# Kernel tuning notes

Hardware: AMD Instinct MI355X
Metric: run time of the kernel (lower is better)

Reference implementation:

```python
import jax, jax.numpy as jnp
import numpy as np

T, B, UNITS, ACTIONS = 128, 16, 128, 6
NORM_SCALE = float(np.sqrt(UNITS))  # norm_scale = sqrt(urnn_units)


def _conv(x, w, b, stride):
    y = jax.lax.conv_general_dilated(x, w, (stride, stride), 'VALID',
                                     dimension_numbers=('NCHW', 'OIHW', 'NCHW'))
    return jax.nn.relu(y + b[None, :, None, None])


def setup_inputs() -> dict:
    key = jax.random.key(0)
    ks = jax.random.split(key, 16)
    rn = lambda k, s, sc=0.05: jax.random.normal(k, s, jnp.float32) * sc
    return {
        'x': jax.random.uniform(ks[0], (T * B, 84, 84, 3), jnp.float32, 0.0, 255.0),
        'done': (jax.random.uniform(ks[1], (T * B,)) < 0.1).astype(jnp.float32),
        'urnn_state_real': jnp.ones((B, UNITS), jnp.float32),
        'urnn_state_imag': jnp.zeros((B, UNITS), jnp.float32),
        'conv1_w': rn(ks[2], (32, 3, 8, 8)), 'conv1_b': jnp.zeros((32,), jnp.float32),
        'conv2_w': rn(ks[3], (64, 32, 4, 4)), 'conv2_b': jnp.zeros((64,), jnp.float32),
        'conv3_w': rn(ks[4], (64, 64, 3, 3)), 'conv3_b': jnp.zeros((64,), jnp.float32),
        'fc_w': rn(ks[5], (3136, 512)), 'fc_b': jnp.zeros((512,), jnp.float32),
        'win_r': rn(ks[6], (512, UNITS)), 'win_i': rn(ks[7], (512, UNITS)),
        'wrec_r': rn(ks[8], (UNITS, UNITS)), 'wrec_i': rn(ks[9], (UNITS, UNITS)),
        'actor_w': rn(ks[10], (2 * UNITS, ACTIONS), 0.01), 'actor_b': jnp.zeros((ACTIONS,), jnp.float32),
        'critic_w': rn(ks[11], (2 * UNITS, 1)), 'critic_b': jnp.zeros((1,), jnp.float32),
    }


def reference(x, done, urnn_state_real, urnn_state_imag,
              conv1_w, conv1_b, conv2_w, conv2_b, conv3_w, conv3_b,
              fc_w, fc_b, win_r, win_i, wrec_r, wrec_i,
              actor_w, actor_b, critic_w, critic_b):
    # CNN backbone (Nature-DQN) on NHWC frames scaled to [0,1]
    h = jnp.transpose(x, (0, 3, 1, 2)) / 255.0
    h = _conv(h, conv1_w, conv1_b, 4)      # [N,32,20,20]
    h = _conv(h, conv2_w, conv2_b, 2)      # [N,64,9,9]
    h = _conv(h, conv3_w, conv3_b, 1)      # [N,64,7,7]
    h = h.reshape(h.shape[0], -1)          # [N,3136]
    h = jax.nn.relu(h @ fc_w + fc_b)       # [N,512]

    h = h.reshape(T, B, -1)
    d = done.reshape(T, B)
    win = win_r + 1j * win_i               # [512,U] complex input projection
    wrec = wrec_r + 1j * wrec_i            # [U,U] complex recurrent matrix
    init = jnp.ones((B, UNITS), jnp.complex64)  # initial_hidden, ||.|| = sqrt(U)
    state0 = (urnn_state_real + 1j * urnn_state_imag).astype(jnp.complex64)

    def step(state, hd):
        ht, dt = hd
        reset = (1.0 - dt)[:, None]
        st = reset * state + (1.0 - reset) * init   # reset-mask blending
        pre = st @ wrec + ht.astype(jnp.complex64) @ win
        norm = jnp.sqrt(jnp.sum(pre.real ** 2 + pre.imag ** 2, axis=-1, keepdims=True))
        new = pre * (NORM_SCALE / norm).astype(jnp.complex64)  # renorm to sqrt(U)
        return new, new

    _, hs = jax.lax.scan(step, state0, (h, d))      # hs: [T,B,U] complex
    hs = hs.reshape(T * B, UNITS)
    hreal = jnp.concatenate([hs.real, hs.imag], axis=-1)  # [T*B, 2U]
    logits = hreal @ actor_w + actor_b
    value = hreal @ critic_w + critic_b
    return jnp.concatenate([logits, value], axis=-1)  # [T*B, ACTIONS+1]
```

## Files before the change

### kernel.cpp

```cpp
#include <hip/hip_runtime.h>
#include <hip/hip_bf16.h>

#define N_FRAMES 2048
#define T_STEPS  128
#define BATCH    16
#define UNITS    128
#define NORM_SCALE 11.313708498984760390f

typedef short bf16x8 __attribute__((ext_vector_type(8)));
typedef float f32x4 __attribute__((ext_vector_type(4)));

static __device__ inline unsigned short f2bf(float f) {
    __hip_bfloat16 h = __float2bfloat16(f);
    return __builtin_bit_cast(unsigned short, h);
}

static const size_t OFF_W1P   = 0;
static const size_t OFF_W2P   = 6144;
static const size_t OFF_W3P   = 38912;
static const size_t OFF_FCWP  = 75776;
static const size_t OFF_HSR   = 1681408;
static const size_t OFF_HSI   = 1943552;
static const size_t OFF_PROJR = 2205696;
static const size_t OFF_PROJI = 2467840;
static const size_t OFF_H     = 2729984;
static const size_t OFF_Y2    = 3778560;
static const size_t OFF_WRTR  = OFF_Y2;
static const size_t OFF_WRTI  = OFF_Y2 + 16384;
static const size_t OFF_Y1    = 14395392;
static const size_t OFF_Y3    = OFF_Y1;

__global__ void permute_w1mf(const float* __restrict__ w, unsigned short* __restrict__ o) {
    int i = blockIdx.x * 256 + threadIdx.x;
    if (i >= 8192) return;
    int j = i & 7; int lane = (i >> 3) & 63; int nt = (i >> 9) & 1; int ky = i >> 10;
    int t = (lane >> 4) * 8 + j;
    int oc = nt * 16 + (lane & 15);
    float v = 0.f;
    if (t < 24) {
        int kx = t / 3, ic = t % 3;
        v = w[((oc * 3 + ic) * 8 + ky) * 8 + kx] * (1.0f / 255.0f);
    }
    o[i] = f2bf(v);
}
__global__ void permute_w2mf(const float* __restrict__ w, unsigned short* __restrict__ o) {
    int i = blockIdx.x * 256 + threadIdx.x;
    if (i >= 32768) return;
    int j = i & 7; int lane = (i >> 3) & 63; int nt = (i >> 9) & 3; int kk = i >> 11;
    int ic = (lane >> 4) * 8 + j;
    int oc = nt * 16 + (lane & 15);
    int ky = kk >> 2, kx = kk & 3;
    o[i] = f2bf(w[((oc * 32 + ic) * 4 + ky) * 4 + kx]);
}
__global__ void permute_w3mf(const float* __restrict__ w, unsigned short* __restrict__ o) {
    int i = blockIdx.x * 256 + threadIdx.x;
    if (i >= 36864) return;
    int j = i & 7; int lane = (i >> 3) & 63; int nt = (i >> 9) & 3; int c = (i >> 11) & 1; int kk = i >> 12;
    int ic = c * 32 + (lane >> 4) * 8 + j;
    int oc = nt * 16 + (lane & 15);
    int ky = kk / 3, kx = kk % 3;
    o[i] = f2bf(w[((oc * 64 + ic) * 3 + ky) * 3 + kx]);
}
__global__ void permute_fcwmf(const float* __restrict__ w, unsigned short* __restrict__ o) {
    int i = blockIdx.x * 256 + threadIdx.x;
    if (i >= 1638400) return;
    int jj = i & 7; int lane = (i >> 3) & 63; int ntg = (i >> 9) & 31; int kk = i >> 14;
    int k = kk * 32 + (lane >> 4) * 8 + jj;
    int n = ntg * 16 + (lane & 15);
    float v = 0.f;
    if (k < 3136) {
        int p = k >> 6, c = k & 63;
        v = w[(size_t)(c * 49 + p) * 512 + n];
    }
    o[i] = f2bf(v);
}
__global__ void permute_wrt(const float* __restrict__ wr, const float* __restrict__ wi,
                            float* __restrict__ otr, float* __restrict__ oti) {
    int i = blockIdx.x * 256 + threadIdx.x;
    if (i >= 16384) return;
    int k = i & 127, u = i >> 7;
    otr[i] = wr[k * 128 + u];
    oti[i] = wi[k * 128 + u];
}

__global__ __launch_bounds__(256) void conv1_kernel(const float* __restrict__ x,
                                                    const unsigned short* __restrict__ wmf,
                                                    const float* __restrict__ b,
                                                    unsigned short* __restrict__ y) {
    __shared__ unsigned short xs[11096];
    int tid = threadIdx.x;
    int blk = blockIdx.x;
    int n = blk >> 1, hb = blk & 1;

    const float4* xb4 = reinterpret_cast<const float4*>(x + (size_t)n * 21168 + hb * 40 * 252);
#pragma unroll
    for (int it = 0; it < 11; ++it) {
        int i = it * 256 + tid;
        if (i < 2772) {
            float4 v = xb4[i];
            ushort4 h;
            h.x = f2bf(v.x); h.y = f2bf(v.y); h.z = f2bf(v.z); h.w = f2bf(v.w);
            *reinterpret_cast<ushort4*>(&xs[i * 4]) = h;
        }
    }
    if (tid < 8) xs[11088 + tid] = 0;
    __syncthreads();

    int lane = tid & 63;
    int wv = tid >> 6;
    int row = lane & 15;
    int seg = lane >> 4;
    const uint4* wm = reinterpret_cast<const uint4*>(wmf);
    float b0 = b[row];
    float b1 = b[16 + row];
    int pbase = n * 400 + hb * 200;

    for (int tile = wv; tile < 13; tile += 4) {
        int p = tile * 16 + row; if (p > 199) p = 199;
        int eb = (p / 20) * 1008 + (p % 20) * 12 + seg * 8;
        f32x4 acc0 = {0.f, 0.f, 0.f, 0.f};
        f32x4 acc1 = {0.f, 0.f, 0.f, 0.f};
#pragma unroll
        for (int ky = 0; ky < 8; ++ky) {
            int ea = eb + ky * 252;
            ushort4 lo = *reinterpret_cast<const ushort4*>(&xs[ea]);
            ushort4 hi = *reinterpret_cast<const ushort4*>(&xs[ea + 4]);
            bf16x8 a = {(short)lo.x, (short)lo.y, (short)lo.z, (short)lo.w,
                        (short)hi.x, (short)hi.y, (short)hi.z, (short)hi.w};
            bf16x8 w0 = __builtin_bit_cast(bf16x8, wm[(ky * 2 + 0) * 64 + lane]);
            bf16x8 w1 = __builtin_bit_cast(bf16x8, wm[(ky * 2 + 1) * 64 + lane]);
            acc0 = __builtin_amdgcn_mfma_f32_16x16x32_bf16(a, w0, acc0, 0, 0, 0);
            acc1 = __builtin_amdgcn_mfma_f32_16x16x32_bf16(a, w1, acc1, 0, 0, 0);
        }
#pragma unroll
        for (int r = 0; r < 4; ++r) {
            int pl = tile * 16 + seg * 4 + r;
            if (pl < 200) {
                unsigned short* yp = y + ((size_t)(pbase + pl)) * 32 + row;
                yp[0]  = f2bf(fmaxf(acc0[r] + b0, 0.f));
                yp[16] = f2bf(fmaxf(acc1[r] + b1, 0.f));
            }
        }
    }
}

__global__ __launch_bounds__(256) void conv2_kernel(const unsigned short* __restrict__ y1b,
                                                    const unsigned short* __restrict__ wt,
                                                    const float* __restrict__ b,
                                                    unsigned short* __restrict__ y2) {
    __shared__ unsigned short xs[2 * 12800];
    int tid = threadIdx.x;
    int n0 = blockIdx.x * 2;
    const uint4* xg = reinterpret_cast<const uint4*>(y1b + (size_t)n0 * 12800);
    uint4* xs4 = reinterpret_cast<uint4*>(xs);
#pragma unroll
    for (int q = 0; q < 13; ++q) {
        int i = q * 256 + tid;
        if (i < 3200) {
            uint4 v = xg[i];
            int swz = (i & ~3) | ((i & 3) ^ ((i >> 3) & 3));
            xs4[swz] = v;
        }
    }
    __syncthreads();

    int lane = tid & 63;
    int wv = tid >> 6;
    int img = wv >> 1;
    int tbase = (wv & 1) * 3;
    int row = lane & 15, seg = lane >> 4;
    int imgb = img * 1600;

    int ibase[3];
#pragma unroll
    for (int t = 0; t < 3; ++t) {
        int p = (tbase + t) * 16 + row; if (p > 80) p = 80;
        ibase[t] = (p / 9) * 40 + (p % 9) * 2;
    }
    const uint4* B4 = reinterpret_cast<const uint4*>(wt);
    f32x4 acc[3][4];
#pragma unroll
    for (int t = 0; t < 3; ++t)
#pragma unroll
        for (int nt = 0; nt < 4; ++nt) acc[t][nt] = (f32x4){0.f, 0.f, 0.f, 0.f};

#pragma unroll 1
    for (int kk = 0; kk < 16; ++kk) {
        int ky = kk >> 2, kx = kk & 3;
        int koff = ky * 20 + kx;
        bf16x8 bb[4];
#pragma unroll
        for (int nt = 0; nt < 4; ++nt)
            bb[nt] = __builtin_bit_cast(bf16x8, B4[(kk * 4 + nt) * 64 + lane]);
        bf16x8 a[3];
#pragma unroll
        for (int t = 0; t < 3; ++t) {
            int ipx = ibase[t] + koff;
            int a16 = imgb + ipx * 4 + (seg ^ ((ipx >> 1) & 3));
            a[t] = __builtin_bit_cast(bf16x8, *reinterpret_cast<const uint4*>(&xs[a16 * 8]));
        }
#pragma unroll
        for (int t = 0; t < 3; ++t)
#pragma unroll
            for (int nt = 0; nt < 4; ++nt)
                acc[t][nt] = __builtin_amdgcn_mfma_f32_16x16x32_bf16(a[t], bb[nt], acc[t][nt], 0, 0, 0);
    }

#pragma unroll
    for (int nt = 0; nt < 4; ++nt) {
        int c = nt * 16 + row;
        float bc = b[c];
#pragma unroll
        for (int t = 0; t < 3; ++t)
#pragma unroll
            for (int r = 0; r < 4; ++r) {
                int p = (tbase + t) * 16 + seg * 4 + r;
                if (p < 81)
                    y2[((size_t)(n0 + img) * 81 + p) * 64 + c] = f2bf(fmaxf(acc[t][nt][r] + bc, 0.f));
            }
    }
}

__global__ __launch_bounds__(256) void conv3_kernel(const unsigned short* __restrict__ y2b,
                                                    const unsigned short* __restrict__ wt,
                                                    const float* __restrict__ b,
                                                    unsigned short* __restrict__ y3) {
    __shared__ unsigned short xs[2 * 5184];
    int tid = threadIdx.x;
    int n0 = blockIdx.x * 2;
    const uint4* xg = reinterpret_cast<const uint4*>(y2b + (size_t)n0 * 5184);
    uint4* xs4 = reinterpret_cast<uint4*>(xs);
#pragma unroll
    for (int q = 0; q < 6; ++q) {
        int i = q * 256 + tid;
        if (i < 1296) {
            uint4 v = xg[i];
            int px = i >> 3, qq = i & 7;
            xs4[px * 8 + (qq ^ (px & 7))] = v;
        }
    }
    __syncthreads();

    int lane = tid & 63;
    int wv = tid >> 6;
    int img = wv >> 1;
    int tbase = (wv & 1) * 2;
    int row = lane & 15, seg = lane >> 4;

    int ibase[2];
#pragma unroll
    for (int t = 0; t < 2; ++t) {
        int p = (tbase + t) * 16 + row; if (p > 48) p = 48;
        ibase[t] = img * 81 + (p / 7) * 9 + (p % 7);
    }
    const uint4* B4 = reinterpret_cast<const uint4*>(wt);
    f32x4 acc[2][4];
#pragma unroll
    for (int t = 0; t < 2; ++t)
#pragma unroll
        for (int nt = 0; nt < 4; ++nt) acc[t][nt] = (f32x4){0.f, 0.f, 0.f, 0.f};

#pragma unroll 1
    for (int kk = 0; kk < 9; ++kk) {
        int ky = kk / 3, kx = kk % 3;
        int koff = ky * 9 + kx;
#pragma unroll
        for (int c = 0; c < 2; ++c) {
            bf16x8 bb[4];
#pragma unroll
            for (int nt = 0; nt < 4; ++nt)
                bb[nt] = __builtin_bit_cast(bf16x8, B4[((kk * 2 + c) * 4 + nt) * 64 + lane]);
            bf16x8 a[2];
#pragma unroll
            for (int t = 0; t < 2; ++t) {
                int px = ibase[t] + koff;
                int u16 = px * 8 + ((c * 4 + seg) ^ (px & 7));
                a[t] = __builtin_bit_cast(bf16x8, *reinterpret_cast<const uint4*>(&xs[u16 * 8]));
            }
#pragma unroll
            for (int t = 0; t < 2; ++t)
#pragma unroll
                for (int nt = 0; nt < 4; ++nt)
                    acc[t][nt] = __builtin_amdgcn_mfma_f32_16x16x32_bf16(a[t], bb[nt], acc[t][nt], 0, 0, 0);
        }
    }

#pragma unroll
    for (int nt = 0; nt < 4; ++nt) {
        int c = nt * 16 + row;
        float bc = b[c];
#pragma unroll
        for (int t = 0; t < 2; ++t)
#pragma unroll
            for (int r = 0; r < 4; ++r) {
                int p = (tbase + t) * 16 + seg * 4 + r;
                if (p < 49)
                    y3[(size_t)(n0 + img) * 3136 + p * 64 + c] = f2bf(fmaxf(acc[t][nt][r] + bc, 0.f));
            }
    }
}

__global__ __launch_bounds__(256) void fc_kernel(const unsigned short* __restrict__ A,
                                                 const unsigned short* __restrict__ Bt,
                                                 const float* __restrict__ bias,
                                                 float* __restrict__ C) {
    __shared__ float Cs[64][65];
    int tid = threadIdx.x;
    int lane = tid & 63;
    int wv = tid >> 6;
    int bm = blockIdx.x & 31;
    int bn = blockIdx.x >> 5;
    int row = lane & 15, seg = lane >> 4;

    const uint4* B4 = reinterpret_cast<const uint4*>(Bt);
    f32x4 acc[4][4];
#pragma unroll
    for (int mf = 0; mf < 4; ++mf)
#pragma unroll
        for (int nf = 0; nf < 4; ++nf) acc[mf][nf] = (f32x4){0.f, 0.f, 0.f, 0.f};

    const unsigned short* Abase = A + (size_t)(bm * 64 + row) * 3136 + seg * 8;

#pragma unroll 1
    for (int kk = wv; kk < 100; kk += 4) {
        bf16x8 a[4], bb[4];
#pragma unroll
        for (int mf = 0; mf < 4; ++mf)
            a[mf] = __builtin_bit_cast(bf16x8,
                *reinterpret_cast<const uint4*>(Abase + (size_t)mf * 16 * 3136 + kk * 32));
#pragma unroll
        for (int nf = 0; nf < 4; ++nf)
            bb[nf] = __builtin_bit_cast(bf16x8, B4[(kk * 32 + bn * 4 + nf) * 64 + lane]);
#pragma unroll
        for (int mf = 0; mf < 4; ++mf)
#pragma unroll
            for (int nf = 0; nf < 4; ++nf)
                acc[mf][nf] = __builtin_amdgcn_mfma_f32_16x16x32_bf16(a[mf], bb[nf], acc[mf][nf], 0, 0, 0);
    }

#pragma unroll 1
    for (int w = 0; w < 4; ++w) {
        if (wv == w) {
#pragma unroll
            for (int mf = 0; mf < 4; ++mf)
#pragma unroll
                for (int nf = 0; nf < 4; ++nf)
#pragma unroll
                    for (int r = 0; r < 4; ++r) {
                        int rr = mf * 16 + seg * 4 + r;
                        int cc = nf * 16 + row;
                        if (w == 0) Cs[rr][cc] = acc[mf][nf][r];
                        else        Cs[rr][cc] += acc[mf][nf][r];
                    }
        }
        __syncthreads();
    }

    int r = tid >> 2, cq = (tid & 3) * 16;
#pragma unroll
    for (int q = 0; q < 4; ++q) {
        int c0 = cq + q * 4;
        float4 v = *reinterpret_cast<float4*>(&Cs[r][c0]);
        float4 bv = *reinterpret_cast<const float4*>(&bias[bn * 64 + c0]);
        v.x = fmaxf(v.x + bv.x, 0.f);
        v.y = fmaxf(v.y + bv.y, 0.f);
        v.z = fmaxf(v.z + bv.z, 0.f);
        v.w = fmaxf(v.w + bv.w, 0.f);
        *reinterpret_cast<float4*>(&C[(size_t)(bm * 64 + r) * 512 + bn * 64 + c0]) = v;
    }
}

__global__ __launch_bounds__(256) void proj_kernel(const float* __restrict__ h,
                                                   const float* __restrict__ winr,
                                                   const float* __restrict__ wini,
                                                   float* __restrict__ pr,
                                                   float* __restrict__ pi) {
    int idx = blockIdx.x * 256 + threadIdx.x;
    int u = idx & 127;
    int n0 = (idx >> 7) * 8;
    float ar[8] = {}, ai[8] = {};
    for (int k = 0; k < 512; ++k) {
        float wrv = winr[k * 128 + u], wiv = wini[k * 128 + u];
#pragma unroll
        for (int g = 0; g < 8; ++g) {
            float hv = h[(size_t)(n0 + g) * 512 + k];
            ar[g] = fmaf(hv, wrv, ar[g]);
            ai[g] = fmaf(hv, wiv, ai[g]);
        }
    }
#pragma unroll
    for (int g = 0; g < 8; ++g) {
        pr[(size_t)(n0 + g) * 128 + u] = ar[g];
        pi[(size_t)(n0 + g) * 128 + u] = ai[g];
    }
}

__global__ __launch_bounds__(512) void scan_kernel(const float* __restrict__ done,
                                                   const float* __restrict__ sr0,
                                                   const float* __restrict__ si0,
                                                   const float* __restrict__ wrtR,
                                                   const float* __restrict__ wrtI,
                                                   const float* __restrict__ pr,
                                                   const float* __restrict__ pi,
                                                   float* __restrict__ hsr,
                                                   float* __restrict__ hsi) {
    int b = blockIdx.x;
    int tid = threadIdx.x;
    int u = tid & 127;
    int s = tid >> 7;
    int w = tid >> 6;

    const float4* wr4 = reinterpret_cast<const float4*>(wrtR + u * 128 + s * 32);
    const float4* wi4 = reinterpret_cast<const float4*>(wrtI + u * 128 + s * 32);
    float4 WR[8], WI[8];
#pragma unroll
    for (int q = 0; q < 8; ++q) { WR[q] = wr4[q]; WI[q] = wi4[q]; }

    __shared__ __align__(16) float stR[128], stI[128];
    __shared__ float parR[4][128], parI[4][128];
    __shared__ float redw[8];

    if (s == 0) { stR[u] = sr0[b * 128 + u]; stI[u] = si0[b * 128 + u]; }
    float cr = 0.f, ci = 0.f;
#pragma unroll
    for (int q = 0; q < 8; ++q) {
        cr += WR[q].x + WR[q].y + WR[q].z + WR[q].w;
        ci += WI[q].x + WI[q].y + WI[q].z + WI[q].w;
    }
    parR[s][u] = cr; parI[s][u] = ci;
    __syncthreads();
    float SWr = parR[0][u] + parR[1][u] + parR[2][u] + parR[3][u];
    float SWi = parI[0][u] + parI[1][u] + parI[2][u] + parI[3][u];
    __syncthreads();

    for (int t = 0; t < T_STEPS; ++t) {
        int np = (t * BATCH + b) * 128 + u;
        float prr = pr[np];
        float pri = pi[np];
        float d = done[t * BATCH + b];
        float r = 1.f - d;

        const float4* sR4 = reinterpret_cast<const float4*>(&stR[s * 32]);
        const float4* sI4 = reinterpret_cast<const float4*>(&stI[s * 32]);
        float ar0 = 0.f, ar1 = 0.f, ai0 = 0.f, ai1 = 0.f;
#pragma unroll
        for (int q = 0; q < 8; ++q) {
            float4 sr = sR4[q], si = sI4[q];
            float4 wrv = WR[q], wiv = WI[q];
            if (q & 1) {
                ar1 = fmaf(sr.x, wrv.x, ar1); ar1 = fmaf(-si.x, wiv.x, ar1);
                ai1 = fmaf(sr.x, wiv.x, ai1); ai1 = fmaf(si.x, wrv.x, ai1);
                ar1 = fmaf(sr.y, wrv.y, ar1); ar1 = fmaf(-si.y, wiv.y, ar1);
                ai1 = fmaf(sr.y, wiv.y, ai1); ai1 = fmaf(si.y, wrv.y, ai1);
                ar1 = fmaf(sr.z, wrv.z, ar1); ar1 = fmaf(-si.z, wiv.z, ar1);
                ai1 = fmaf(sr.z, wiv.z, ai1); ai1 = fmaf(si.z, wrv.z, ai1);
                ar1 = fmaf(sr.w, wrv.w, ar1); ar1 = fmaf(-si.w, wiv.w, ar1);
                ai1 = fmaf(sr.w, wiv.w, ai1); ai1 = fmaf(si.w, wrv.w, ai1);
            } else {
                ar0 = fmaf(sr.x, wrv.x, ar0); ar0 = fmaf(-si.x, wiv.x, ar0);
                ai0 = fmaf(sr.x, wiv.x, ai0); ai0 = fmaf(si.x, wrv.x, ai0);
                ar0 = fmaf(sr.y, wrv.y, ar0); ar0 = fmaf(-si.y, wiv.y, ar0);
                ai0 = fmaf(sr.y, wiv.y, ai0); ai0 = fmaf(si.y, wrv.y, ai0);
                ar0 = fmaf(sr.z, wrv.z, ar0); ar0 = fmaf(-si.z, wiv.z, ar0);
                ai0 = fmaf(sr.z, wiv.z, ai0); ai0 = fmaf(si.z, wrv.z, ai0);
                ar0 = fmaf(sr.w, wrv.w, ar0); ar0 = fmaf(-si.w, wiv.w, ar0);
                ai0 = fmaf(sr.w, wiv.w, ai0); ai0 = fmaf(si.w, wrv.w, ai0);
            }
        }
        parR[s][u] = ar0 + ar1;
        parI[s][u] = ai0 + ai1;
        __syncthreads();

        float tr_ = (parR[0][u] + parR[1][u]) + (parR[2][u] + parR[3][u]);
        float ti_ = (parI[0][u] + parI[1][u]) + (parI[2][u] + parI[3][u]);
        float pre_r = fmaf(r, tr_, fmaf(d, SWr, prr));
        float pre_i = fmaf(r, ti_, fmaf(d, SWi, pri));
        float sq = fmaf(pre_r, pre_r, pre_i * pre_i);
#pragma unroll
        for (int off = 32; off; off >>= 1) sq += __shfl_xor(sq, off);
        if ((tid & 63) == 0) redw[w] = sq;
        __syncthreads();

        float norm = redw[s * 2] + redw[s * 2 + 1];
        float scale = NORM_SCALE / sqrtf(norm);
        float nr = pre_r * scale, ni = pre_i * scale;
        if (s == 0) {
            stR[u] = nr; stI[u] = ni;
            hsr[np] = nr; hsi[np] = ni;
        }
        __syncthreads();
    }
}

__global__ void heads_kernel(const float* __restrict__ hsr, const float* __restrict__ hsi,
                             const float* __restrict__ aw, const float* __restrict__ ab,
                             const float* __restrict__ cw, const float* __restrict__ cb,
                             float* __restrict__ out) {
    int idx = blockIdx.x * 256 + threadIdx.x;
    if (idx >= N_FRAMES * 7) return;
    int j = idx % 7;
    int n = idx / 7;
    float acc;
    if (j < 6) {
        acc = ab[j];
        for (int k = 0; k < 128; ++k) acc = fmaf(hsr[n * 128 + k], aw[k * 6 + j], acc);
        for (int k = 0; k < 128; ++k) acc = fmaf(hsi[n * 128 + k], aw[(128 + k) * 6 + j], acc);
    } else {
        acc = cb[0];
        for (int k = 0; k < 128; ++k) acc = fmaf(hsr[n * 128 + k], cw[k], acc);
        for (int k = 0; k < 128; ++k) acc = fmaf(hsi[n * 128 + k], cw[128 + k], acc);
    }
    out[idx] = acc;
}

extern "C" void kernel_launch(void* const* d_in, const int* in_sizes, int n_in,
                              void* d_out, int out_size, void* d_ws, size_t ws_size,
                              hipStream_t stream) {
    const float* x        = (const float*)d_in[0];
    const float* done     = (const float*)d_in[1];
    const float* sr0      = (const float*)d_in[2];
    const float* si0      = (const float*)d_in[3];
    const float* conv1_w  = (const float*)d_in[4];
    const float* conv1_b  = (const float*)d_in[5];
    const float* conv2_w  = (const float*)d_in[6];
    const float* conv2_b  = (const float*)d_in[7];
    const float* conv3_w  = (const float*)d_in[8];
    const float* conv3_b  = (const float*)d_in[9];
    const float* fc_w     = (const float*)d_in[10];
    const float* fc_b     = (const float*)d_in[11];
    const float* win_r    = (const float*)d_in[12];
    const float* win_i    = (const float*)d_in[13];
    const float* wrec_r   = (const float*)d_in[14];
    const float* wrec_i   = (const float*)d_in[15];
    const float* actor_w  = (const float*)d_in[16];
    const float* actor_b  = (const float*)d_in[17];
    const float* critic_w = (const float*)d_in[18];
    const float* critic_b = (const float*)d_in[19];

    float* ws = (float*)d_ws;
    unsigned short* w1mf = (unsigned short*)(ws + OFF_W1P);
    unsigned short* w2mf = (unsigned short*)(ws + OFF_W2P);
    unsigned short* w3mf = (unsigned short*)(ws + OFF_W3P);
    unsigned short* fcb = (unsigned short*)(ws + OFF_FCWP);
    float* hsr  = ws + OFF_HSR;
    float* hsi  = ws + OFF_HSI;
    float* prj  = ws + OFF_PROJR;
    float* pij  = ws + OFF_PROJI;
    float* h    = ws + OFF_H;
    unsigned short* y2b = (unsigned short*)(ws + OFF_Y2);
    float* wrtR = ws + OFF_WRTR;
    float* wrtI = ws + OFF_WRTI;
    unsigned short* y1b = (unsigned short*)(ws + OFF_Y1);
    unsigned short* y3b = (unsigned short*)(ws + OFF_Y3);
    float* outp = (float*)d_out;

    hipLaunchKernelGGL(permute_w1mf, dim3(32), dim3(256), 0, stream, conv1_w, w1mf);
    hipLaunchKernelGGL(permute_w2mf, dim3(128), dim3(256), 0, stream, conv2_w, w2mf);
    hipLaunchKernelGGL(permute_w3mf, dim3(144), dim3(256), 0, stream, conv3_w, w3mf);
    hipLaunchKernelGGL(permute_fcwmf, dim3(6400), dim3(256), 0, stream, fc_w, fcb);

    hipLaunchKernelGGL(conv1_kernel, dim3(4096), dim3(256), 0, stream, x, w1mf, conv1_b, y1b);
    hipLaunchKernelGGL(conv2_kernel, dim3(1024), dim3(256), 0, stream, y1b, w2mf, conv2_b, y2b);
    hipLaunchKernelGGL(conv3_kernel, dim3(1024), dim3(256), 0, stream, y2b, w3mf, conv3_b, y3b);
    hipLaunchKernelGGL(permute_wrt, dim3(64), dim3(256), 0, stream, wrec_r, wrec_i, wrtR, wrtI);
    hipLaunchKernelGGL(fc_kernel, dim3(256), dim3(256), 0, stream, y3b, fcb, fc_b, h);
    hipLaunchKernelGGL(proj_kernel, dim3(128), dim3(256), 0, stream, h, win_r, win_i, prj, pij);
    hipLaunchKernelGGL(scan_kernel, dim3(16), dim3(512), 0, stream,
                       done, sr0, si0, wrtR, wrtI, prj, pij, hsr, hsi);
    hipLaunchKernelGGL(heads_kernel, dim3(56), dim3(256), 0, stream,
                       hsr, hsi, actor_w, actor_b, critic_w, critic_b, outp);
}
```

Measured before the change: 374.3 us.

## Run recurrent scan for all batches in one block using bf16 MFMA

Replaces the per-batch fp32 FMA scan (16 blocks) with a single 512-thread block that computes all 16 batch rows per step as a 16x128x128 complex matmul via bf16 MFMA, keeping the recurrent weights in registers and the state in swizzled LDS. Reset blending and next-step projection loads are folded into the previous step's epilogue so they overlap with compute. Projections and hidden states are stored interleaved as float2. This cuts per-step FMA latency on the serial critical path, but it lowers state precision to bf16 and runs on only one CU.

```diff
diff --git a/kernel.cpp b/kernel.cpp
--- a/kernel.cpp
+++ b/kernel.cpp
@@ -19,14 +19,11 @@
 static const size_t OFF_W2P   = 6144;
 static const size_t OFF_W3P   = 38912;
 static const size_t OFF_FCWP  = 75776;
+static const size_t OFF_WSC   = 894976;
 static const size_t OFF_HSR   = 1681408;
-static const size_t OFF_HSI   = 1943552;
 static const size_t OFF_PROJR = 2205696;
-static const size_t OFF_PROJI = 2467840;
 static const size_t OFF_H     = 2729984;
 static const size_t OFF_Y2    = 3778560;
-static const size_t OFF_WRTR  = OFF_Y2;
-static const size_t OFF_WRTI  = OFF_Y2 + 16384;
 static const size_t OFF_Y1    = 14395392;
 static const size_t OFF_Y3    = OFF_Y1;
 
@@ -74,13 +71,16 @@
     }
     o[i] = f2bf(v);
 }
-__global__ void permute_wrt(const float* __restrict__ wr, const float* __restrict__ wi,
-                            float* __restrict__ otr, float* __restrict__ oti) {
+__global__ void permute_wscan(const float* __restrict__ wr, const float* __restrict__ wi,
+                              unsigned short* __restrict__ o) {
     int i = blockIdx.x * 256 + threadIdx.x;
-    if (i >= 16384) return;
-    int k = i & 127, u = i >> 7;
-    otr[i] = wr[k * 128 + u];
-    oti[i] = wi[k * 128 + u];
+    if (i >= 32768) return;
+    int j = i & 7; int lane = (i >> 3) & 63; int ks = (i >> 9) & 3; int nt = (i >> 11) & 7;
+    int comp = i >> 14;
+    int k = ks * 32 + (lane >> 4) * 8 + j;
+    int n = nt * 16 + (lane & 15);
+    const float* src = comp ? wi : wr;
+    o[i] = f2bf(src[k * 128 + n]);
 }
 
 __global__ __launch_bounds__(256) void conv1_kernel(const float* __restrict__ x,
@@ -373,8 +373,7 @@
 __global__ __launch_bounds__(256) void proj_kernel(const float* __restrict__ h,
                                                    const float* __restrict__ winr,
                                                    const float* __restrict__ wini,
-                                                   float* __restrict__ pr,
-                                                   float* __restrict__ pi) {
+                                                   float2* __restrict__ pj) {
     int idx = blockIdx.x * 256 + threadIdx.x;
     int u = idx & 127;
     int n0 = (idx >> 7) * 8;
@@ -389,110 +388,129 @@
         }
     }
 #pragma unroll
-    for (int g = 0; g < 8; ++g) {
-        pr[(size_t)(n0 + g) * 128 + u] = ar[g];
-        pi[(size_t)(n0 + g) * 128 + u] = ai[g];
-    }
-}
-
-__global__ __launch_bounds__(512) void scan_kernel(const float* __restrict__ done,
-                                                   const float* __restrict__ sr0,
-                                                   const float* __restrict__ si0,
-                                                   const float* __restrict__ wrtR,
-                                                   const float* __restrict__ wrtI,
-                                                   const float* __restrict__ pr,
-                                                   const float* __restrict__ pi,
-                                                   float* __restrict__ hsr,
-                                                   float* __restrict__ hsi) {
-    int b = blockIdx.x;
+    for (int g = 0; g < 8; ++g)
+        pj[(size_t)(n0 + g) * 128 + u] = make_float2(ar[g], ai[g]);
+}
+
+__global__ __launch_bounds__(512, 2) void scan_kernel(const float* __restrict__ done,
+                                                      const float* __restrict__ sr0,
+                                                      const float* __restrict__ si0,
+                                                      const unsigned short* __restrict__ wsc,
+                                                      const float2* __restrict__ pj,
+                                                      float2* __restrict__ hs) {
+    __shared__ __align__(16) unsigned short stR[2048], stI[2048];
+    __shared__ __align__(16) float npart[16][8];
     int tid = threadIdx.x;
-    int u = tid & 127;
-    int s = tid >> 7;
-    int w = tid >> 6;
-
-    const float4* wr4 = reinterpret_cast<const float4*>(wrtR + u * 128 + s * 32);
-    const float4* wi4 = reinterpret_cast<const float4*>(wrtI + u * 128 + s * 32);
-    float4 WR[8], WI[8];
-#pragma unroll
-    for (int q = 0; q < 8; ++q) { WR[q] = wr4[q]; WI[q] = wi4[q]; }
-
-    __shared__ __align__(16) float stR[128], stI[128];
-    __shared__ float parR[4][128], parI[4][128];
-    __shared__ float redw[8];
-
-    if (s == 0) { stR[u] = sr0[b * 128 + u]; stI[u] = si0[b * 128 + u]; }
-    float cr = 0.f, ci = 0.f;
-#pragma unroll
-    for (int q = 0; q < 8; ++q) {
-        cr += WR[q].x + WR[q].y + WR[q].z + WR[q].w;
-        ci += WI[q].x + WI[q].y + WI[q].z + WI[q].w;
-    }
-    parR[s][u] = cr; parI[s][u] = ci;
+    int lane = tid & 63, wv = tid >> 6;
+    int row = lane & 15, seg = lane >> 4;
+    int u = wv * 16 + row;
+
+    const uint4* W4 = reinterpret_cast<const uint4*>(wsc);
+    bf16x8 WR[4], WI[4];
+#pragma unroll
+    for (int ks = 0; ks < 4; ++ks) {
+        WR[ks] = __builtin_bit_cast(bf16x8, W4[((0 * 8 + wv) * 4 + ks) * 64 + lane]);
+        WI[ks] = __builtin_bit_cast(bf16x8, W4[((1 * 8 + wv) * 4 + ks) * 64 + lane]);
+    }
+
+    for (int e = tid; e < 2048; e += 512) {
+        int uu = e & 127, b = e >> 7;
+        float d = done[b];
+        float sr = sr0[b * 128 + uu], si = si0[b * 128 + uu];
+        float bsr = (1.f - d) * sr + d;
+        float bsi = (1.f - d) * si;
+        int sw = ((uu >> 3) ^ (b & 15));
+        stR[b * 128 + sw * 8 + (uu & 7)] = f2bf(bsr);
+        stI[b * 128 + sw * 8 + (uu & 7)] = f2bf(bsi);
+    }
     __syncthreads();
-    float SWr = parR[0][u] + parR[1][u] + parR[2][u] + parR[3][u];
-    float SWi = parI[0][u] + parI[1][u] + parI[2][u] + parI[3][u];
-    __syncthreads();
+
+    float2 pjc[4];
+#pragma unroll
+    for (int r = 0; r < 4; ++r) {
+        int b = seg * 4 + r;
+        pjc[r] = pj[(size_t)(0 * 16 + b) * 128 + u];
+    }
 
     for (int t = 0; t < T_STEPS; ++t) {
-        int np = (t * BATCH + b) * 128 + u;
-        float prr = pr[np];
-        float pri = pi[np];
-        float d = done[t * BATCH + b];
-        float r = 1.f - d;
-
-        const float4* sR4 = reinterpret_cast<const float4*>(&stR[s * 32]);
-        const float4* sI4 = reinterpret_cast<const float4*>(&stI[s * 32]);
-        float ar0 = 0.f, ar1 = 0.f, ai0 = 0.f, ai1 = 0.f;
-#pragma unroll
-        for (int q = 0; q < 8; ++q) {
-            float4 sr = sR4[q], si = sI4[q];
-            float4 wrv = WR[q], wiv = WI[q];
-            if (q & 1) {
-                ar1 = fmaf(sr.x, wrv.x, ar1); ar1 = fmaf(-si.x, wiv.x, ar1);
-                ai1 = fmaf(sr.x, wiv.x, ai1); ai1 = fmaf(si.x, wrv.x, ai1);
-                ar1 = fmaf(sr.y, wrv.y, ar1); ar1 = fmaf(-si.y, wiv.y, ar1);
-                ai1 = fmaf(sr.y, wiv.y, ai1); ai1 = fmaf(si.y, wrv.y, ai1);
-                ar1 = fmaf(sr.z, wrv.z, ar1); ar1 = fmaf(-si.z, wiv.z, ar1);
-                ai1 = fmaf(sr.z, wiv.z, ai1); ai1 = fmaf(si.z, wrv.z, ai1);
-                ar1 = fmaf(sr.w, wrv.w, ar1); ar1 = fmaf(-si.w, wiv.w, ar1);
-                ai1 = fmaf(sr.w, wiv.w, ai1); ai1 = fmaf(si.w, wrv.w, ai1);
-            } else {
-                ar0 = fmaf(sr.x, wrv.x, ar0); ar0 = fmaf(-si.x, wiv.x, ar0);
-                ai0 = fmaf(sr.x, wiv.x, ai0); ai0 = fmaf(si.x, wrv.x, ai0);
-                ar0 = fmaf(sr.y, wrv.y, ar0); ar0 = fmaf(-si.y, wiv.y, ar0);
-                ai0 = fmaf(sr.y, wiv.y, ai0); ai0 = fmaf(si.y, wrv.y, ai0);
-                ar0 = fmaf(sr.z, wrv.z, ar0); ar0 = fmaf(-si.z, wiv.z, ar0);
-                ai0 = fmaf(sr.z, wiv.z, ai0); ai0 = fmaf(si.z, wrv.z, ai0);
-                ar0 = fmaf(sr.w, wrv.w, ar0); ar0 = fmaf(-si.w, wiv.w, ar0);
-                ai0 = fmaf(sr.w, wiv.w, ai0); ai0 = fmaf(si.w, wrv.w, ai0);
-            }
-        }
-        parR[s][u] = ar0 + ar1;
-        parI[s][u] = ai0 + ai1;
+        float2 pjn[4];
+        float dn[4];
+        int tn = (t + 1 < T_STEPS) ? t + 1 : 127;
+#pragma unroll
+        for (int r = 0; r < 4; ++r) {
+            int b = seg * 4 + r;
+            pjn[r] = pj[(size_t)(tn * 16 + b) * 128 + u];
+            dn[r] = (t + 1 < T_STEPS) ? done[(t + 1) * 16 + b] : 0.f;
+        }
+
+        bf16x8 aR[4], aI[4], aIn[4];
+#pragma unroll
+        for (int ks = 0; ks < 4; ++ks) {
+            int unit = (ks * 4 + seg) ^ row;
+            aR[ks] = __builtin_bit_cast(bf16x8,
+                *reinterpret_cast<const uint4*>(&stR[row * 128 + unit * 8]));
+            uint4 vi = *reinterpret_cast<const uint4*>(&stI[row * 128 + unit * 8]);
+            aI[ks] = __builtin_bit_cast(bf16x8, vi);
+            uint4 vn = {vi.x ^ 0x80008000u, vi.y ^ 0x80008000u,
+                        vi.z ^ 0x80008000u, vi.w ^ 0x80008000u};
+            aIn[ks] = __builtin_bit_cast(bf16x8, vn);
+        }
+
+        f32x4 accR = {0.f, 0.f, 0.f, 0.f};
+        f32x4 accI = {0.f, 0.f, 0.f, 0.f};
+#pragma unroll
+        for (int ks = 0; ks < 4; ++ks) {
+            accR = __builtin_amdgcn_mfma_f32_16x16x32_bf16(aR[ks], WR[ks], accR, 0, 0, 0);
+            accR = __builtin_amdgcn_mfma_f32_16x16x32_bf16(aIn[ks], WI[ks], accR, 0, 0, 0);
+            accI = __builtin_amdgcn_mfma_f32_16x16x32_bf16(aR[ks], WI[ks], accI, 0, 0, 0);
+            accI = __builtin_amdgcn_mfma_f32_16x16x32_bf16(aI[ks], WR[ks], accI, 0, 0, 0);
+        }
+
+        float prer[4], prei[4], sq[4];
+#pragma unroll
+        for (int r = 0; r < 4; ++r) {
+            prer[r] = accR[r] + pjc[r].x;
+            prei[r] = accI[r] + pjc[r].y;
+            sq[r] = fmaf(prer[r], prer[r], prei[r] * prei[r]);
+        }
+#pragma unroll
+        for (int off = 1; off <= 8; off <<= 1) {
+#pragma unroll
+            for (int r = 0; r < 4; ++r) sq[r] += __shfl_xor(sq[r], off);
+        }
+        if (row == 0) {
+#pragma unroll
+            for (int r = 0; r < 4; ++r) npart[seg * 4 + r][wv] = sq[r];
+        }
         __syncthreads();
 
-        float tr_ = (parR[0][u] + parR[1][u]) + (parR[2][u] + parR[3][u]);
-        float ti_ = (parI[0][u] + parI[1][u]) + (parI[2][u] + parI[3][u]);
-        float pre_r = fmaf(r, tr_, fmaf(d, SWr, prr));
-        float pre_i = fmaf(r, ti_, fmaf(d, SWi, pri));
-        float sq = fmaf(pre_r, pre_r, pre_i * pre_i);
-#pragma unroll
-        for (int off = 32; off; off >>= 1) sq += __shfl_xor(sq, off);
-        if ((tid & 63) == 0) redw[w] = sq;
+        float scale[4];
+#pragma unroll
+        for (int r = 0; r < 4; ++r) {
+            const float4* np4 = reinterpret_cast<const float4*>(&npart[seg * 4 + r][0]);
+            float4 n0 = np4[0], n1 = np4[1];
+            float nm = ((n0.x + n0.y) + (n0.z + n0.w)) + ((n1.x + n1.y) + (n1.z + n1.w));
+            scale[r] = NORM_SCALE * rsqrtf(nm);
+        }
+#pragma unroll
+        for (int r = 0; r < 4; ++r) {
+            int b = seg * 4 + r;
+            float nr = prer[r] * scale[r];
+            float ni = prei[r] * scale[r];
+            hs[(size_t)(t * 16 + b) * 128 + u] = make_float2(nr, ni);
+            float bsr = (1.f - dn[r]) * nr + dn[r];
+            float bsi = (1.f - dn[r]) * ni;
+            int sw = ((u >> 3) ^ (b & 15));
+            stR[b * 128 + sw * 8 + (u & 7)] = f2bf(bsr);
+            stI[b * 128 + sw * 8 + (u & 7)] = f2bf(bsi);
+        }
         __syncthreads();
-
-        float norm = redw[s * 2] + redw[s * 2 + 1];
-        float scale = NORM_SCALE / sqrtf(norm);
-        float nr = pre_r * scale, ni = pre_i * scale;
-        if (s == 0) {
-            stR[u] = nr; stI[u] = ni;
-            hsr[np] = nr; hsi[np] = ni;
-        }
-        __syncthreads();
-    }
-}
-
-__global__ void heads_kernel(const float* __restrict__ hsr, const float* __restrict__ hsi,
+#pragma unroll
+        for (int r = 0; r < 4; ++r) pjc[r] = pjn[r];
+    }
+}
+
+__global__ void heads_kernel(const float2* __restrict__ hs,
                              const float* __restrict__ aw, const float* __restrict__ ab,
                              const float* __restrict__ cw, const float* __restrict__ cb,
                              float* __restrict__ out) {
@@ -500,15 +518,22 @@
     if (idx >= N_FRAMES * 7) return;
     int j = idx % 7;
     int n = idx / 7;
+    const float2* hp = hs + (size_t)n * 128;
     float acc;
     if (j < 6) {
         acc = ab[j];
-        for (int k = 0; k < 128; ++k) acc = fmaf(hsr[n * 128 + k], aw[k * 6 + j], acc);
-        for (int k = 0; k < 128; ++k) acc = fmaf(hsi[n * 128 + k], aw[(128 + k) * 6 + j], acc);
+        for (int k = 0; k < 128; ++k) {
+            float2 v = hp[k];
+            acc = fmaf(v.x, aw[k * 6 + j], acc);
+            acc = fmaf(v.y, aw[(128 + k) * 6 + j], acc);
+        }
     } else {
         acc = cb[0];
-        for (int k = 0; k < 128; ++k) acc = fmaf(hsr[n * 128 + k], cw[k], acc);
-        for (int k = 0; k < 128; ++k) acc = fmaf(hsi[n * 128 + k], cw[128 + k], acc);
+        for (int k = 0; k < 128; ++k) {
+            float2 v = hp[k];
+            acc = fmaf(v.x, cw[k], acc);
+            acc = fmaf(v.y, cw[128 + k], acc);
+        }
     }
     out[idx] = acc;
 }
@@ -542,14 +567,11 @@
     unsigned short* w2mf = (unsigned short*)(ws + OFF_W2P);
     unsigned short* w3mf = (unsigned short*)(ws + OFF_W3P);
     unsigned short* fcb = (unsigned short*)(ws + OFF_FCWP);
-    float* hsr  = ws + OFF_HSR;
-    float* hsi  = ws + OFF_HSI;
-    float* prj  = ws + OFF_PROJR;
-    float* pij  = ws + OFF_PROJI;
+    unsigned short* wsc = (unsigned short*)(ws + OFF_WSC);
+    float2* hs  = (float2*)(ws + OFF_HSR);
+    float2* pj  = (float2*)(ws + OFF_PROJR);
     float* h    = ws + OFF_H;
     unsigned short* y2b = (unsigned short*)(ws + OFF_Y2);
-    float* wrtR = ws + OFF_WRTR;
-    float* wrtI = ws + OFF_WRTI;
     unsigned short* y1b = (unsigned short*)(ws + OFF_Y1);
     unsigned short* y3b = (unsigned short*)(ws + OFF_Y3);
     float* outp = (float*)d_out;
@@ -558,15 +580,15 @@
     hipLaunchKernelGGL(permute_w2mf, dim3(128), dim3(256), 0, stream, conv2_w, w2mf);
     hipLaunchKernelGGL(permute_w3mf, dim3(144), dim3(256), 0, stream, conv3_w, w3mf);
     hipLaunchKernelGGL(permute_fcwmf, dim3(6400), dim3(256), 0, stream, fc_w, fcb);
+    hipLaunchKernelGGL(permute_wscan, dim3(128), dim3(256), 0, stream, wrec_r, wrec_i, wsc);
 
     hipLaunchKernelGGL(conv1_kernel, dim3(4096), dim3(256), 0, stream, x, w1mf, conv1_b, y1b);
     hipLaunchKernelGGL(conv2_kernel, dim3(1024), dim3(256), 0, stream, y1b, w2mf, conv2_b, y2b);
     hipLaunchKernelGGL(conv3_kernel, dim3(1024), dim3(256), 0, stream, y2b, w3mf, conv3_b, y3b);
-    hipLaunchKernelGGL(permute_wrt, dim3(64), dim3(256), 0, stream, wrec_r, wrec_i, wrtR, wrtI);
     hipLaunchKernelGGL(fc_kernel, dim3(256), dim3(256), 0, stream, y3b, fcb, fc_b, h);
-    hipLaunchKernelGGL(proj_kernel, dim3(128), dim3(256), 0, stream, h, win_r, win_i, prj, pij);
-    hipLaunchKernelGGL(scan_kernel, dim3(16), dim3(512), 0, stream,
-                       done, sr0, si0, wrtR, wrtI, prj, pij, hsr, hsi);
+    hipLaunchKernelGGL(proj_kernel, dim3(128), dim3(256), 0, stream, h, win_r, win_i, pj);
+    hipLaunchKernelGGL(scan_kernel, dim3(1), dim3(512), 0, stream,
+                       done, sr0, si0, wsc, pj, hs);
     hipLaunchKernelGGL(heads_kernel, dim3(56), dim3(256), 0, stream,
-                       hsr, hsi, actor_w, actor_b, critic_w, critic_b, outp);
-}
+                       hs, actor_w, actor_b, critic_w, critic_b, outp);
+}
```

New measurement: 407.4 us. +8.8%, slower.
